# Performance work log

Measured on AMD Instinct MI355X. Metric: run time of the kernel, lower is better.

## Reference

```python
import jax, jax.numpy as jnp
import numpy as np

# module hyperparameters (match init_kwargs)
D_IN = 32
N_BAND_IN = 32
D_OUT = 32
K_BAND = 4
K_T = 3
DIL_T = 1
STRIDE_B = 2
PAD_B = 1
PAD_B_OUT = 0

# derived band geometry (same formulas as ConvTranspose2dBandPadder)
N_UP = (N_BAND_IN - 1) * STRIDE_B + 1            # zero-interleaved bands
PAD_TOP = K_BAND - 1 - PAD_B
PAD_BOT = PAD_TOP + PAD_B_OUT
N_PADDED = N_UP + PAD_TOP + PAD_BOT              # bands fed to the conv
N_BAND_OUT = N_PADDED - K_BAND + 1               # valid conv along bands

B = 8
T = 1000


def setup_inputs() -> dict:
    key = jax.random.key(0)
    k1, k2, k3 = jax.random.split(key, 3)
    x = jax.random.normal(k1, (B, D_IN * N_BAND_IN, T), jnp.float32)
    W = jax.random.normal(k2, (D_OUT, D_IN, K_BAND, K_T), jnp.float32) * 0.05
    b = jax.random.normal(k3, (D_OUT,), jnp.float32) * 0.05
    return {"x": x, "W": W, "b": b}


def reference(x, W, b):
    """x: (B, D_IN*N_BAND_IN, T) band-major channels -> (B, D_OUT*N_BAND_OUT, T)."""
    Bs, _, Ts = x.shape
    # chunk(dim=1, n_band_in): band-major layout (band, feature)
    bands = x.reshape(Bs, N_BAND_IN, D_IN, Ts)
    # zero-interleave bands by stride + top/bottom zero-band padding
    up = jnp.zeros((Bs, N_PADDED, D_IN, Ts), x.dtype)
    up = up.at[:, PAD_TOP:PAD_TOP + N_UP:STRIDE_B].set(bands)
    # 2D conv: channels = D_IN, spatial = (band, time), causal in time
    xin = up.transpose(0, 2, 1, 3)  # (B, D_IN, N_PADDED, T)
    pad_t = (K_T - 1) * DIL_T
    y = jax.lax.conv_general_dilated(
        xin, W,
        window_strides=(1, 1),
        padding=((0, 0), (pad_t, 0)),  # valid over bands, causal over time
        rhs_dilation=(1, DIL_T),
        dimension_numbers=("NCHW", "OIHW", "NCHW"),
    )  # (B, D_OUT, N_BAND_OUT, T)
    y = y + b[None, :, None, None]
    # back to band-major flattened channels
    return y.transpose(0, 2, 1, 3).reshape(Bs, D_OUT * N_BAND_OUT, Ts)
```

## Files before the change

kernel.cpp:

```cpp
#include <hip/hip_runtime.h>
#include <cstddef>
#include <cstdint>


typedef __bf16 bf16x8 __attribute__((ext_vector_type(8)));
typedef __bf16 bf16x4 __attribute__((ext_vector_type(4)));
typedef float  f32x4  __attribute__((ext_vector_type(4)));

#define D_IN_ 32
#define D_OUT_ 32
#define N_BI_ 32
#define N_BO_ 64
#define K_B_ 4
#define K_T_ 3
#define T_ 1000
#define B_ 8

#define TT_ 252
#define XROWS_ 260
#define ROWB_ 64
#define WT_ELEMS (2 * 6 * 2 * 64 * 8)

__device__ __forceinline__ int swz(int t) { return (t & 3) ^ ((t >> 2) & 3); }

__global__ __launch_bounds__(256)
void wprep(const float* __restrict__ W, __bf16* __restrict__ wt) {
    int idx = blockIdx.x * 256 + threadIdx.x;
    if (idx >= WT_ELEMS) return;
    int r = idx & 7, l = (idx >> 3) & 63, mt = (idx >> 9) & 1, rest = idx >> 10;
    int ks = rest % 6, p = rest / 6;
    int dout = mt * 16 + (l & 15), din = (l >> 4) * 8 + r;
    int j = ks / 3, kt = ks % 3, kb = 2 * j + p;
    wt[idx] = (__bf16)W[((dout * D_IN_ + din) * K_B_ + kb) * K_T_ + kt];
}

__global__ __launch_bounds__(512)
void tct_pair(const float* __restrict__ x, const __bf16* __restrict__ wt,
              const float* __restrict__ bias, float* __restrict__ out)
{
    __shared__ unsigned char xl[2 * XROWS_ * ROWB_];

    const int tid = threadIdx.x;
    const int l   = tid & 63;
    const int w   = tid >> 6;
    const int mt  = w >> 2;
    const int wq  = w & 3;
    const int tl  = l & 15;
    const int cch = l >> 4;
    const int k   = (int)blockIdx.y - 1;
    const int bb  = blockIdx.z;
    const int t0  = blockIdx.x * TT_;

    bf16x8 afrag[2][6];
    {
        const bf16x8* wp = (const bf16x8*)wt;
#pragma unroll
        for (int p = 0; p < 2; ++p)
#pragma unroll
            for (int ks = 0; ks < 6; ++ks)
                afrag[p][ks] = wp[p * 768 + ks * 128 + mt * 64 + l];
    }

    {
        const int g  = tid >> 4;
        const int u  = tid & 15;
        const int si = u >> 3;
        const int dg = u & 7;
        const int s  = k + si;
        const bool bandok = (s >= 0) && (s < N_BI_);
        const float* xb = x + ((size_t)(bb * N_BI_ + (bandok ? s : 0)) * D_IN_ + dg * 4) * T_;
        unsigned char* lbase = xl + si * (XROWS_ * ROWB_);
        const int c = dg >> 1, h = dg & 1;

        f32x4 vv[2][4];
        bool ok[2];
#pragma unroll
        for (int it = 0; it < 2; ++it) {
            const int tg = t0 - 4 + (g + it * 32) * 4;
            ok[it] = bandok && (tg >= 0) && (tg < T_);
#pragma unroll
            for (int i = 0; i < 4; ++i)
                vv[it][i] = ok[it] ? *(const f32x4*)(xb + (size_t)i * T_ + tg)
                                   : (f32x4){0.f, 0.f, 0.f, 0.f};
        }
#pragma unroll
        for (int it = 0; it < 2; ++it) {
            const int tq = g + it * 32;
#pragma unroll
            for (int kk = 0; kk < 4; ++kk) {
                const int t = tq * 4 + kk;
                bf16x4 row;
                row[0] = (__bf16)vv[it][0][kk];
                row[1] = (__bf16)vv[it][1][kk];
                row[2] = (__bf16)vv[it][2][kk];
                row[3] = (__bf16)vv[it][3][kk];
                *(bf16x4*)(lbase + t * ROWB_ + ((c ^ swz(t)) << 4) + (h << 3)) = row;
            }
        }
    }
    __syncthreads();

    f32x4 acc[2][4];
#pragma unroll
    for (int p = 0; p < 2; ++p)
#pragma unroll
        for (int nt = 0; nt < 4; ++nt)
#pragma unroll
            for (int r = 0; r < 4; ++r) acc[p][nt][r] = 0.f;

#pragma unroll
    for (int nt = 0; nt < 4; ++nt) {
#pragma unroll
        for (int j = 0; j < 2; ++j) {
            const unsigned char* xbnd = xl + j * (XROWS_ * ROWB_);
#pragma unroll
            for (int kt = 0; kt < 3; ++kt) {
                const int lt = wq * 64 + nt * 16 + tl + kt + 2;
                const bf16x8 bfrag = *(const bf16x8*)(xbnd + lt * ROWB_
                                                      + ((cch ^ swz(lt)) << 4));
                const int ks = j * 3 + kt;
                acc[0][nt] = __builtin_amdgcn_mfma_f32_16x16x32_bf16(afrag[0][ks], bfrag, acc[0][nt], 0, 0, 0);
                acc[1][nt] = __builtin_amdgcn_mfma_f32_16x16x32_bf16(afrag[1][ks], bfrag, acc[1][nt], 0, 0, 0);
            }
        }
    }

    const int rbase = cch * 4;
    float bv[4];
#pragma unroll
    for (int r = 0; r < 4; ++r) bv[r] = bias[mt * 16 + rbase + r];

#pragma unroll
    for (int p = 0; p < 2; ++p) {
        const int n = 2 * k + 2 - p;
        if (n < 0 || n >= N_BO_) continue;
        float* opb = out + ((size_t)(bb * N_BO_ + n) * D_OUT_ + mt * 16 + rbase) * T_;
#pragma unroll
        for (int nt = 0; nt < 4; ++nt) {
            const int lcol = wq * 64 + nt * 16 + tl;
            const int tcol = t0 + lcol;
            if (lcol < TT_ && tcol < T_) {
#pragma unroll
                for (int r = 0; r < 4; ++r)
                    opb[(size_t)r * T_ + tcol] = acc[p][nt][r] + bv[r];
            }
        }
    }
}

__global__ __launch_bounds__(256)
void tct_fallback(const float* __restrict__ x, const float* __restrict__ W,
                  const float* __restrict__ bias, float* __restrict__ out)
{
    const int lane = threadIdx.x & 63;
    const int wav  = __builtin_amdgcn_readfirstlane(threadIdx.x >> 6);
    const int dog  = wav * 8;
    const int n    = blockIdx.y;
    const int bb   = blockIdx.z;
    const int p    = n & 1;
    int t0 = blockIdx.x * 256 + lane * 4;
    const bool act = (t0 < T_);
    if (!act) t0 = T_ - 4;
    float acc[8][4];
#pragma unroll
    for (int i = 0; i < 8; ++i)
#pragma unroll
        for (int u = 0; u < 4; ++u) acc[i][u] = 0.f;
#pragma unroll
    for (int j = 0; j < 2; ++j) {
        const int s = (n + 2 * j + p - 2) >> 1;
        if (s < 0 || s >= N_BI_) continue;
        const int kb = 2 * j + p;
        const float* xband = x + (size_t)(bb * N_BI_ + s) * D_IN_ * T_;
        for (int d_in = 0; d_in < D_IN_; ++d_in) {
            const float* xr = xband + d_in * T_;
            const float4 xc = *(const float4*)(xr + t0);
            float4 xp = make_float4(0.f, 0.f, 0.f, 0.f);
            if (t0 > 0) xp = *(const float4*)(xr + t0 - 4);
            const float xv[6] = {xp.z, xp.w, xc.x, xc.y, xc.z, xc.w};
#pragma unroll
            for (int kt = 0; kt < K_T_; ++kt) {
                float wv[8];
#pragma unroll
                for (int i = 0; i < 8; ++i) {
                    const int widx = __builtin_amdgcn_readfirstlane(
                        (((dog + i) * D_IN_ + d_in) * K_B_ + kb) * K_T_ + kt);
                    wv[i] = W[widx];
                }
#pragma unroll
                for (int i = 0; i < 8; ++i)
#pragma unroll
                    for (int u = 0; u < 4; ++u)
                        acc[i][u] = fmaf(wv[i], xv[u + kt], acc[i][u]);
            }
        }
    }
    if (act) {
        float bvv[8];
#pragma unroll
        for (int i = 0; i < 8; ++i) bvv[i] = bias[dog + i];
        float* op = out + ((size_t)(bb * N_BO_ + n) * D_OUT_ + dog) * T_ + t0;
#pragma unroll
        for (int i = 0; i < 8; ++i) {
            float4 v;
            v.x = acc[i][0] + bvv[i]; v.y = acc[i][1] + bvv[i];
            v.z = acc[i][2] + bvv[i]; v.w = acc[i][3] + bvv[i];
            *(float4*)(op + (size_t)i * T_) = v;
        }
    }
}

extern "C" void kernel_launch(void* const* d_in, const int* in_sizes, int n_in,
                              void* d_out, int out_size, void* d_ws, size_t ws_size,
                              hipStream_t stream) {
    const float* x    = (const float*)d_in[0];
    const float* W    = (const float*)d_in[1];
    const float* bias = (const float*)d_in[2];
    float* out = (float*)d_out;

    if (ws_size >= (size_t)WT_ELEMS * sizeof(__bf16)) {
        __bf16* wt = (__bf16*)d_ws;
        wprep<<<(WT_ELEMS + 255) / 256, 256, 0, stream>>>(W, wt);
        dim3 grid((T_ + TT_ - 1) / TT_, N_BO_ / 2 + 1, B_);
        tct_pair<<<grid, dim3(512), 0, stream>>>(x, wt, bias, out);
    } else {
        tct_fallback<<<dim3((T_ + 255) / 256, N_BO_, B_), dim3(256), 0, stream>>>(x, W, bias, out);
    }
}
```

Measured before the change: 110.9 us.

## Double time tile per workgroup, flatten grid, and overlap weight loads with staging

Each workgroup now covers 500 time steps instead of 252, so the grid shrinks from 4x33x8 to 2x33x8 blocks, flattened to 1D with batch as the fastest index. The 4-column halo overlap is paid fewer times and the weight fragments are loaded once per larger tile. Weight and bias loads move after the LDS staging stores and before the barrier, and the MFMA/store loop runs in two chunks to limit accumulator registers. LDS use doubles (64 KB) and launch_bounds requests 2 blocks per CU, which may add register pressure. Fewer blocks (528) may also leave the mi355x's CUs less evenly loaded.

```diff
diff --git a/kernel.cpp b/kernel.cpp
--- a/kernel.cpp
+++ b/kernel.cpp
@@ -16,8 +16,8 @@
 #define T_ 1000
 #define B_ 8
 
-#define TT_ 252
-#define XROWS_ 260
+#define TT_ 500
+#define XR_ 512
 #define ROWB_ 64
 #define WT_ELEMS (2 * 6 * 2 * 64 * 8)
 
@@ -34,11 +34,19 @@
     wt[idx] = (__bf16)W[((dout * D_IN_ + din) * K_B_ + kb) * K_T_ + kt];
 }
 
-__global__ __launch_bounds__(512)
+__global__ __launch_bounds__(512, 2)
 void tct_pair(const float* __restrict__ x, const __bf16* __restrict__ wt,
               const float* __restrict__ bias, float* __restrict__ out)
 {
-    __shared__ unsigned char xl[2 * XROWS_ * ROWB_];
+    __shared__ unsigned char xl[2 * XR_ * ROWB_];
+
+    const int wg  = blockIdx.x;
+    const int bb  = wg & 7;
+    const int rr  = wg >> 3;
+    const int kk  = rr >> 1;
+    const int th  = rr & 1;
+    const int k   = kk - 1;
+    const int t0  = th * TT_;
 
     const int tid = threadIdx.x;
     const int l   = tid & 63;
@@ -47,19 +55,6 @@
     const int wq  = w & 3;
     const int tl  = l & 15;
     const int cch = l >> 4;
-    const int k   = (int)blockIdx.y - 1;
-    const int bb  = blockIdx.z;
-    const int t0  = blockIdx.x * TT_;
-
-    bf16x8 afrag[2][6];
-    {
-        const bf16x8* wp = (const bf16x8*)wt;
-#pragma unroll
-        for (int p = 0; p < 2; ++p)
-#pragma unroll
-            for (int ks = 0; ks < 6; ++ks)
-                afrag[p][ks] = wp[p * 768 + ks * 128 + mt * 64 + l];
-    }
 
     {
         const int g  = tid >> 4;
@@ -69,60 +64,43 @@
         const int s  = k + si;
         const bool bandok = (s >= 0) && (s < N_BI_);
         const float* xb = x + ((size_t)(bb * N_BI_ + (bandok ? s : 0)) * D_IN_ + dg * 4) * T_;
-        unsigned char* lbase = xl + si * (XROWS_ * ROWB_);
+        unsigned char* lbase = xl + si * (XR_ * ROWB_);
         const int c = dg >> 1, h = dg & 1;
 
-        f32x4 vv[2][4];
-        bool ok[2];
-#pragma unroll
-        for (int it = 0; it < 2; ++it) {
+        f32x4 vv[4][4];
+#pragma unroll
+        for (int it = 0; it < 4; ++it) {
             const int tg = t0 - 4 + (g + it * 32) * 4;
-            ok[it] = bandok && (tg >= 0) && (tg < T_);
+            const bool ok = bandok && (tg >= 0) && (tg < T_);
 #pragma unroll
             for (int i = 0; i < 4; ++i)
-                vv[it][i] = ok[it] ? *(const f32x4*)(xb + (size_t)i * T_ + tg)
-                                   : (f32x4){0.f, 0.f, 0.f, 0.f};
-        }
-#pragma unroll
-        for (int it = 0; it < 2; ++it) {
+                vv[it][i] = ok ? *(const f32x4*)(xb + (size_t)i * T_ + tg)
+                               : (f32x4){0.f, 0.f, 0.f, 0.f};
+        }
+#pragma unroll
+        for (int it = 0; it < 4; ++it) {
             const int tq = g + it * 32;
 #pragma unroll
-            for (int kk = 0; kk < 4; ++kk) {
-                const int t = tq * 4 + kk;
+            for (int e = 0; e < 4; ++e) {
+                const int t = tq * 4 + e;
                 bf16x4 row;
-                row[0] = (__bf16)vv[it][0][kk];
-                row[1] = (__bf16)vv[it][1][kk];
-                row[2] = (__bf16)vv[it][2][kk];
-                row[3] = (__bf16)vv[it][3][kk];
+                row[0] = (__bf16)vv[it][0][e];
+                row[1] = (__bf16)vv[it][1][e];
+                row[2] = (__bf16)vv[it][2][e];
+                row[3] = (__bf16)vv[it][3][e];
                 *(bf16x4*)(lbase + t * ROWB_ + ((c ^ swz(t)) << 4) + (h << 3)) = row;
             }
         }
     }
-    __syncthreads();
-
-    f32x4 acc[2][4];
-#pragma unroll
-    for (int p = 0; p < 2; ++p)
-#pragma unroll
-        for (int nt = 0; nt < 4; ++nt)
-#pragma unroll
-            for (int r = 0; r < 4; ++r) acc[p][nt][r] = 0.f;
-
-#pragma unroll
-    for (int nt = 0; nt < 4; ++nt) {
-#pragma unroll
-        for (int j = 0; j < 2; ++j) {
-            const unsigned char* xbnd = xl + j * (XROWS_ * ROWB_);
-#pragma unroll
-            for (int kt = 0; kt < 3; ++kt) {
-                const int lt = wq * 64 + nt * 16 + tl + kt + 2;
-                const bf16x8 bfrag = *(const bf16x8*)(xbnd + lt * ROWB_
-                                                      + ((cch ^ swz(lt)) << 4));
-                const int ks = j * 3 + kt;
-                acc[0][nt] = __builtin_amdgcn_mfma_f32_16x16x32_bf16(afrag[0][ks], bfrag, acc[0][nt], 0, 0, 0);
-                acc[1][nt] = __builtin_amdgcn_mfma_f32_16x16x32_bf16(afrag[1][ks], bfrag, acc[1][nt], 0, 0, 0);
-            }
-        }
+
+    bf16x8 afrag[2][6];
+    {
+        const bf16x8* wp = (const bf16x8*)wt;
+#pragma unroll
+        for (int p = 0; p < 2; ++p)
+#pragma unroll
+            for (int ks = 0; ks < 6; ++ks)
+                afrag[p][ks] = wp[p * 768 + ks * 128 + mt * 64 + l];
     }
 
     const int rbase = cch * 4;
@@ -130,19 +108,50 @@
 #pragma unroll
     for (int r = 0; r < 4; ++r) bv[r] = bias[mt * 16 + rbase + r];
 
-#pragma unroll
-    for (int p = 0; p < 2; ++p) {
-        const int n = 2 * k + 2 - p;
-        if (n < 0 || n >= N_BO_) continue;
-        float* opb = out + ((size_t)(bb * N_BO_ + n) * D_OUT_ + mt * 16 + rbase) * T_;
-#pragma unroll
-        for (int nt = 0; nt < 4; ++nt) {
-            const int lcol = wq * 64 + nt * 16 + tl;
-            const int tcol = t0 + lcol;
-            if (lcol < TT_ && tcol < T_) {
-#pragma unroll
-                for (int r = 0; r < 4; ++r)
-                    opb[(size_t)r * T_ + tcol] = acc[p][nt][r] + bv[r];
+    __syncthreads();
+
+#pragma unroll
+    for (int ntc = 0; ntc < 2; ++ntc) {
+        f32x4 acc[2][4];
+#pragma unroll
+        for (int p = 0; p < 2; ++p)
+#pragma unroll
+            for (int n4 = 0; n4 < 4; ++n4)
+#pragma unroll
+                for (int r = 0; r < 4; ++r) acc[p][n4][r] = 0.f;
+
+#pragma unroll
+        for (int n4 = 0; n4 < 4; ++n4) {
+            const int nt = ntc * 4 + n4;
+#pragma unroll
+            for (int j = 0; j < 2; ++j) {
+                const unsigned char* xbnd = xl + j * (XR_ * ROWB_);
+#pragma unroll
+                for (int kt = 0; kt < 3; ++kt) {
+                    const int lt = (wq * 128 + nt * 16 + tl + kt + 2) & (XR_ - 1);
+                    const bf16x8 bfrag = *(const bf16x8*)(xbnd + lt * ROWB_
+                                                          + ((cch ^ swz(lt)) << 4));
+                    const int ks = j * 3 + kt;
+                    acc[0][n4] = __builtin_amdgcn_mfma_f32_16x16x32_bf16(afrag[0][ks], bfrag, acc[0][n4], 0, 0, 0);
+                    acc[1][n4] = __builtin_amdgcn_mfma_f32_16x16x32_bf16(afrag[1][ks], bfrag, acc[1][n4], 0, 0, 0);
+                }
+            }
+        }
+
+#pragma unroll
+        for (int p = 0; p < 2; ++p) {
+            const int n = 2 * k + 2 - p;
+            if (n < 0 || n >= N_BO_) continue;
+            float* opb = out + ((size_t)(bb * N_BO_ + n) * D_OUT_ + mt * 16 + rbase) * T_;
+#pragma unroll
+            for (int n4 = 0; n4 < 4; ++n4) {
+                const int lcol = wq * 128 + (ntc * 4 + n4) * 16 + tl;
+                if (lcol < TT_) {
+                    const int tcol = t0 + lcol;
+#pragma unroll
+                    for (int r = 0; r < 4; ++r)
+                        opb[(size_t)r * T_ + tcol] = acc[p][n4][r] + bv[r];
+                }
             }
         }
     }
@@ -221,8 +230,7 @@
     if (ws_size >= (size_t)WT_ELEMS * sizeof(__bf16)) {
         __bf16* wt = (__bf16*)d_ws;
         wprep<<<(WT_ELEMS + 255) / 256, 256, 0, stream>>>(W, wt);
-        dim3 grid((T_ + TT_ - 1) / TT_, N_BO_ / 2 + 1, B_);
-        tct_pair<<<grid, dim3(512), 0, stream>>>(x, wt, bias, out);
+        tct_pair<<<dim3(8 * 33 * 2), dim3(512), 0, stream>>>(x, wt, bias, out);
     } else {
         tct_fallback<<<dim3((T_ + 255) / 256, N_BO_, B_), dim3(256), 0, stream>>>(x, W, bias, out);
     }
```

Measured after the change: 106.1 us. -4.3%, faster.
